# Optimization experiments

Measured on AMD Instinct MI355X. Metric: run time of the kernel, lower is better.

## Reference

```python
import jax, jax.numpy as jnp
import numpy as np

B, C, D = 1024, 1000, 256
EPS = 1e-4


def setup_inputs() -> dict:
    key = jax.random.key(0)
    k_z, k_mu = jax.random.split(key)
    z = jax.random.normal(k_z, (B, D), dtype=jnp.float32)
    mu = jax.random.normal(k_mu, (C, D), dtype=jnp.float32)  # init.normal_(mu, 0, 1)
    prior_logits = jnp.zeros((C,), dtype=jnp.float32)          # init.zeros_
    precision_factor = jnp.eye(D, dtype=jnp.float32)           # init.eye_
    return {"z": z, "mu": mu, "prior_logits": prior_logits,
            "precision_factor": precision_factor}


def reference(z, mu, prior_logits, precision_factor):
    # Shared precision matrix: symmetrized F F^T + eps I  -> (D, D)
    precision = precision_factor @ precision_factor.T
    precision = 0.5 * (precision + precision.T)
    precision = precision + EPS * jnp.eye(D, dtype=precision_factor.dtype)

    log_prior = jax.nn.log_softmax(prior_logits)  # (C,)

    # Mahalanobis distance per (sample, class): (z-mu)^T P (z-mu)
    diff = z[:, None, :] - mu[None, :, :]                      # (B, C, D)
    m2 = jnp.einsum('bcd,de,bce->bc', diff, precision, diff)   # (B, C)

    return log_prior[None, :] - 0.5 * m2
```

## Files before the change

### kernel.cpp

```cpp
#include <hip/hip_runtime.h>
#include <hip/hip_bf16.h>
#include <math.h>

constexpr int Bn = 1024;
constexpr int Cn = 1000;
constexpr int Dn = 256;
constexpr float EPS = 1e-4f;

typedef __attribute__((ext_vector_type(8))) short bf16x8;
typedef __attribute__((ext_vector_type(4))) float f32x4;

static __device__ __forceinline__ unsigned short f2bf(float x) {
    union { float f; unsigned u; } v; v.f = x;
    return (unsigned short)((v.u + 0x7fffu + ((v.u >> 16) & 1u)) >> 16);
}
static __device__ __forceinline__ float bf2f(unsigned short h) {
    union { unsigned u; float f; } v; v.u = ((unsigned)h) << 16; return v.f;
}
static __device__ __forceinline__ bf16x8 cvt8(const float4 lo, const float4 hi) {
    bf16x8 r;
    r[0] = (short)f2bf(lo.x); r[1] = (short)f2bf(lo.y);
    r[2] = (short)f2bf(lo.z); r[3] = (short)f2bf(lo.w);
    r[4] = (short)f2bf(hi.x); r[5] = (short)f2bf(hi.y);
    r[6] = (short)f2bf(hi.z); r[7] = (short)f2bf(hi.w);
    return r;
}

__global__ __launch_bounds__(256) void w_kernel(const float* __restrict__ z,
                                                const float* __restrict__ mu,
                                                const float* __restrict__ logits,
                                                const float* __restrict__ F,
                                                unsigned short* __restrict__ Wb,
                                                float* __restrict__ epsn,
                                                float* __restrict__ lse_p) {
    const int bid = blockIdx.x, tid = threadIdx.x;

    if (bid == 256) {
        __shared__ float rl[256];
        float mx = -INFINITY;
        for (int i = tid; i < Cn; i += 256) mx = fmaxf(mx, logits[i]);
        rl[tid] = mx; __syncthreads();
        for (int s = 128; s > 0; s >>= 1) {
            if (tid < s) rl[tid] = fmaxf(rl[tid], rl[tid + s]);
            __syncthreads();
        }
        mx = rl[0]; __syncthreads();
        float sm = 0.f;
        for (int i = tid; i < Cn; i += 256) sm += expf(logits[i] - mx);
        rl[tid] = sm; __syncthreads();
        for (int s = 128; s > 0; s >>= 1) {
            if (tid < s) rl[tid] += rl[tid + s];
            __syncthreads();
        }
        if (tid == 0) *lse_p = mx + logf(rl[0]);
        return;
    }

    const int row0 = (bid >> 3) * 64;
    const int col0 = (bid & 7) * 32;
    const int lane = tid & 63, w = tid >> 6;
    const int wr = (w >> 1) * 32, wc = (w & 1) * 16;
    const int la = lane & 15, kg = lane >> 4;

    const int g0 = row0 + wr + la;
    const int g1 = g0 + 16;
    const float* arow0 = (g0 < 1024) ? &z[(size_t)g0 * Dn]
                                     : &mu[(size_t)min(g0 - 1024, Cn - 1) * Dn];
    const float* arow1 = (g1 < 1024) ? &z[(size_t)g1 * Dn]
                                     : &mu[(size_t)min(g1 - 1024, Cn - 1) * Dn];
    const int bcol = col0 + wc + la;

    f32x4 acc0 = {0.f, 0.f, 0.f, 0.f};
    f32x4 acc1 = {0.f, 0.f, 0.f, 0.f};

#pragma unroll
    for (int kt = 0; kt < 8; ++kt) {
        const int k0 = kt * 32 + kg * 8;
        const float4 a0lo = *(const float4*)&arow0[k0];
        const float4 a0hi = *(const float4*)&arow0[k0 + 4];
        const float4 a1lo = *(const float4*)&arow1[k0];
        const float4 a1hi = *(const float4*)&arow1[k0 + 4];
        bf16x8 b0;
#pragma unroll
        for (int j = 0; j < 8; ++j)
            b0[j] = (short)f2bf(F[(size_t)(k0 + j) * Dn + bcol]);
        const bf16x8 a0 = cvt8(a0lo, a0hi);
        const bf16x8 a1 = cvt8(a1lo, a1hi);
        acc0 = __builtin_amdgcn_mfma_f32_16x16x32_bf16(a0, b0, acc0, 0, 0, 0);
        acc1 = __builtin_amdgcn_mfma_f32_16x16x32_bf16(a1, b0, acc1, 0, 0, 0);
    }

    const int rb0 = row0 + wr + kg * 4;
#pragma unroll
    for (int j = 0; j < 4; ++j) {
        Wb[(size_t)(rb0 + j) * Dn + bcol]      = f2bf(acc0[j]);
        Wb[(size_t)(rb0 + 16 + j) * Dn + bcol] = f2bf(acc1[j]);
    }

    if (col0 == 0) {
        __shared__ float red[64][4];
        const int r = tid >> 2, q = tid & 3;
        const int g = row0 + r;
        const float* src = (g < 1024) ? &z[(size_t)g * Dn]
                                      : &mu[(size_t)min(g - 1024, Cn - 1) * Dn];
        const float4* p4 = (const float4*)&src[q << 6];
        float s = 0.f;
#pragma unroll
        for (int i = 0; i < 16; ++i) {
            const float4 v = p4[i];
            s += v.x * v.x + v.y * v.y + v.z * v.z + v.w * v.w;
        }
        red[r][q] = s;
        __syncthreads();
        if (tid < 64)
            epsn[row0 + tid] = EPS * (red[tid][0] + red[tid][1] +
                                      red[tid][2] + red[tid][3]);
    }
}

__global__ __launch_bounds__(256) void main_kernel(const unsigned short* __restrict__ Wb,
                                                   const float* __restrict__ epsn,
                                                   const float* __restrict__ logits,
                                                   const float* __restrict__ lse_p,
                                                   float* __restrict__ out) {
    __shared__ float red[64][4];
    __shared__ float rowbias[64], colbias[64];
    const int bid = blockIdx.x, tid = threadIdx.x;
    const int row0 = (bid >> 4) * 64;
    const int col0 = (bid & 15) * 64;
    const int r = tid >> 2, q = tid & 3;

    {
        const bf16x8* py = (const bf16x8*)&Wb[(size_t)(row0 + r) * Dn + (q << 6)];
        float s = 0.f;
#pragma unroll
        for (int i = 0; i < 8; ++i) {
            const bf16x8 h = py[i];
#pragma unroll
            for (int j = 0; j < 8; ++j) {
                const float f = bf2f((unsigned short)h[j]);
                s = fmaf(f, f, s);
            }
        }
        red[r][q] = s;
    }
    __syncthreads();
    if (tid < 64)
        rowbias[tid] = -0.5f * (red[tid][0] + red[tid][1] + red[tid][2] +
                                red[tid][3] + epsn[row0 + tid]);
    __syncthreads();
    {
        const bf16x8* pu = (const bf16x8*)&Wb[(size_t)(1024 + col0 + r) * Dn + (q << 6)];
        float s = 0.f;
#pragma unroll
        for (int i = 0; i < 8; ++i) {
            const bf16x8 h = pu[i];
#pragma unroll
            for (int j = 0; j < 8; ++j) {
                const float f = bf2f((unsigned short)h[j]);
                s = fmaf(f, f, s);
            }
        }
        red[r][q] = s;
    }
    __syncthreads();
    if (tid < 64) {
        const int c = col0 + tid;
        colbias[tid] = (c < Cn)
            ? logits[c] - *lse_p - 0.5f * (red[tid][0] + red[tid][1] + red[tid][2] +
                                           red[tid][3] + epsn[1024 + c])
            : 0.f;
    }
    __syncthreads();

    const int lane = tid & 63, w = tid >> 6;
    const int wr = (w >> 1) * 32, wc = (w & 1) * 32;
    const int la = lane & 15, kg = lane >> 4;

    const bf16x8* pa = (const bf16x8*)&Wb[(size_t)(row0 + wr + la) * Dn + kg * 8];
    const bf16x8* pb = (const bf16x8*)&Wb[(size_t)(1024 + col0 + wc + la) * Dn + kg * 8];

    f32x4 acc00 = {0.f, 0.f, 0.f, 0.f};
    f32x4 acc01 = {0.f, 0.f, 0.f, 0.f};
    f32x4 acc10 = {0.f, 0.f, 0.f, 0.f};
    f32x4 acc11 = {0.f, 0.f, 0.f, 0.f};

#pragma unroll
    for (int kt = 0; kt < 8; ++kt) {
        const bf16x8 a0 = pa[kt * 4];
        const bf16x8 a1 = pa[kt * 4 + 512];
        const bf16x8 b0 = pb[kt * 4];
        const bf16x8 b1 = pb[kt * 4 + 512];
        acc00 = __builtin_amdgcn_mfma_f32_16x16x32_bf16(a0, b0, acc00, 0, 0, 0);
        acc01 = __builtin_amdgcn_mfma_f32_16x16x32_bf16(a0, b1, acc01, 0, 0, 0);
        acc10 = __builtin_amdgcn_mfma_f32_16x16x32_bf16(a1, b0, acc10, 0, 0, 0);
        acc11 = __builtin_amdgcn_mfma_f32_16x16x32_bf16(a1, b1, acc11, 0, 0, 0);
    }

    const int rbase = kg * 4;
#define EPI(ACC, RF, CF)                                                        \
    do {                                                                        \
        const int gcl = wc + (CF)*16 + la;                                      \
        const int gc  = col0 + gcl;                                             \
        if (gc < Cn) {                                                          \
            const float cb = colbias[gcl];                                      \
            _Pragma("unroll")                                                   \
            for (int j = 0; j < 4; ++j) {                                       \
                const int rlc = wr + (RF)*16 + rbase + j;                       \
                out[(size_t)(row0 + rlc) * Cn + gc] = ACC[j] + rowbias[rlc] + cb; \
            }                                                                   \
        }                                                                       \
    } while (0)

    EPI(acc00, 0, 0); EPI(acc01, 0, 1); EPI(acc10, 1, 0); EPI(acc11, 1, 1);
#undef EPI
}

extern "C" void kernel_launch(void* const* d_in, const int* in_sizes, int n_in,
                              void* d_out, int out_size, void* d_ws, size_t ws_size,
                              hipStream_t stream) {
    const float* z      = (const float*)d_in[0];
    const float* mu     = (const float*)d_in[1];
    const float* logits = (const float*)d_in[2];
    const float* F      = (const float*)d_in[3];
    float* out = (float*)d_out;

    char* ws = (char*)d_ws;
    unsigned short* Wb = (unsigned short*)(ws);
    float* epsn = (float*)(ws + (1 << 20));
    float* lse  = epsn + 2048;

    w_kernel<<<dim3(257), dim3(256), 0, stream>>>(z, mu, logits, F, Wb, epsn, lse);
    main_kernel<<<dim3(256), dim3(256), 0, stream>>>(Wb, epsn, logits, lse, out);
}
```

Measured before the change: 21.44 us.

## Fuse W projection and distance GEMM into one kernel with swizzled LDS tiles

Merges the two-kernel pipeline into a single kernel. Each block loads its 64 z rows and 64 mu rows into XOR-swizzled LDS as bf16, projects both through F into LDS, computes the row and column norms, and runs the final MFMA GEMM from LDS. This removes the second launch, the workspace round trip, and the global sync between stages. In exchange, every block recomputes the F projections and the log-sum-exp redundantly, reading all of F, and uses about 130KB of LDS, which limits occupancy to one block per CU.

```diff
diff --git a/kernel.cpp b/kernel.cpp
--- a/kernel.cpp
+++ b/kernel.cpp
@@ -17,26 +17,33 @@
 static __device__ __forceinline__ float bf2f(unsigned short h) {
     union { unsigned u; float f; } v; v.u = ((unsigned)h) << 16; return v.f;
 }
-static __device__ __forceinline__ bf16x8 cvt8(const float4 lo, const float4 hi) {
-    bf16x8 r;
-    r[0] = (short)f2bf(lo.x); r[1] = (short)f2bf(lo.y);
-    r[2] = (short)f2bf(lo.z); r[3] = (short)f2bf(lo.w);
-    r[4] = (short)f2bf(hi.x); r[5] = (short)f2bf(hi.y);
-    r[6] = (short)f2bf(hi.z); r[7] = (short)f2bf(hi.w);
-    return r;
-}
-
-__global__ __launch_bounds__(256) void w_kernel(const float* __restrict__ z,
-                                                const float* __restrict__ mu,
-                                                const float* __restrict__ logits,
-                                                const float* __restrict__ F,
-                                                unsigned short* __restrict__ Wb,
-                                                float* __restrict__ epsn,
-                                                float* __restrict__ lse_p) {
+
+static __device__ __forceinline__ unsigned short* lds_u(unsigned short* base, int row, int b) {
+    return (unsigned short*)((char*)base + row * 512 + (b ^ ((row & 7) << 4)));
+}
+static __device__ __forceinline__ const unsigned short* lds_c(const unsigned short* base, int row, int b) {
+    return (const unsigned short*)((const char*)base + row * 512 + (b ^ ((row & 7) << 4)));
+}
+
+__global__ __launch_bounds__(256) void lda_one_kernel(const float* __restrict__ z,
+                                                      const float* __restrict__ mu,
+                                                      const float* __restrict__ logits,
+                                                      const float* __restrict__ F,
+                                                      float* __restrict__ out) {
+    __shared__ unsigned short Zl[64 * 256];
+    __shared__ unsigned short Ml[64 * 256];
+    __shared__ unsigned short Yl[64 * 256];
+    __shared__ unsigned short Ul[64 * 256];
+    __shared__ float red[64][4];
+    __shared__ float rowbias[64], colbias[64];
+    __shared__ float rl[256];
+    __shared__ float lse_s;
+
     const int bid = blockIdx.x, tid = threadIdx.x;
-
-    if (bid == 256) {
-        __shared__ float rl[256];
+    const int row0 = (bid >> 4) * 64;
+    const int col0 = (bid & 15) * 64;
+
+    {
         float mx = -INFINITY;
         for (int i = tid; i < Cn; i += 256) mx = fmaxf(mx, logits[i]);
         rl[tid] = mx; __syncthreads();
@@ -52,133 +59,117 @@
             if (tid < s) rl[tid] += rl[tid + s];
             __syncthreads();
         }
-        if (tid == 0) *lse_p = mx + logf(rl[0]);
-        return;
-    }
-
-    const int row0 = (bid >> 3) * 64;
-    const int col0 = (bid & 7) * 32;
+        if (tid == 0) lse_s = mx + logf(rl[0]);
+    }
+
+#pragma unroll
+    for (int i = 0; i < 16; ++i) {
+        const int flat = i * 256 + tid;
+        const int r = flat >> 6, c4 = flat & 63;
+        const float4 vz = *(const float4*)&z[(size_t)(row0 + r) * Dn + c4 * 4];
+        ushort4 sz;
+        sz.x = f2bf(vz.x); sz.y = f2bf(vz.y); sz.z = f2bf(vz.z); sz.w = f2bf(vz.w);
+        *(ushort4*)lds_u(Zl, r, c4 * 8) = sz;
+        const int rm = min(col0 + r, Cn - 1);
+        const float4 vm = *(const float4*)&mu[(size_t)rm * Dn + c4 * 4];
+        ushort4 smv;
+        smv.x = f2bf(vm.x); smv.y = f2bf(vm.y); smv.z = f2bf(vm.z); smv.w = f2bf(vm.w);
+        *(ushort4*)lds_u(Ml, r, c4 * 8) = smv;
+    }
+    __syncthreads();
+
     const int lane = tid & 63, w = tid >> 6;
-    const int wr = (w >> 1) * 32, wc = (w & 1) * 16;
     const int la = lane & 15, kg = lane >> 4;
 
-    const int g0 = row0 + wr + la;
-    const int g1 = g0 + 16;
-    const float* arow0 = (g0 < 1024) ? &z[(size_t)g0 * Dn]
-                                     : &mu[(size_t)min(g0 - 1024, Cn - 1) * Dn];
-    const float* arow1 = (g1 < 1024) ? &z[(size_t)g1 * Dn]
-                                     : &mu[(size_t)min(g1 - 1024, Cn - 1) * Dn];
-    const int bcol = col0 + wc + la;
-
-    f32x4 acc0 = {0.f, 0.f, 0.f, 0.f};
-    f32x4 acc1 = {0.f, 0.f, 0.f, 0.f};
-
-#pragma unroll
-    for (int kt = 0; kt < 8; ++kt) {
-        const int k0 = kt * 32 + kg * 8;
-        const float4 a0lo = *(const float4*)&arow0[k0];
-        const float4 a0hi = *(const float4*)&arow0[k0 + 4];
-        const float4 a1lo = *(const float4*)&arow1[k0];
-        const float4 a1hi = *(const float4*)&arow1[k0 + 4];
-        bf16x8 b0;
-#pragma unroll
-        for (int j = 0; j < 8; ++j)
-            b0[j] = (short)f2bf(F[(size_t)(k0 + j) * Dn + bcol]);
-        const bf16x8 a0 = cvt8(a0lo, a0hi);
-        const bf16x8 a1 = cvt8(a1lo, a1hi);
-        acc0 = __builtin_amdgcn_mfma_f32_16x16x32_bf16(a0, b0, acc0, 0, 0, 0);
-        acc1 = __builtin_amdgcn_mfma_f32_16x16x32_bf16(a1, b0, acc1, 0, 0, 0);
-    }
-
-    const int rb0 = row0 + wr + kg * 4;
-#pragma unroll
-    for (int j = 0; j < 4; ++j) {
-        Wb[(size_t)(rb0 + j) * Dn + bcol]      = f2bf(acc0[j]);
-        Wb[(size_t)(rb0 + 16 + j) * Dn + bcol] = f2bf(acc1[j]);
-    }
-
-    if (col0 == 0) {
-        __shared__ float red[64][4];
+    {
+        const int wr = (w >> 1) * 32, wc = (w & 1) * 16;
+#pragma unroll 1
+        for (int ct = 0; ct < 8; ++ct) {
+            const int bcol = ct * 32 + wc + la;
+            bf16x8 ball[8];
+#pragma unroll
+            for (int kt = 0; kt < 8; ++kt) {
+                const int k0 = kt * 32 + kg * 8;
+                float bf[8];
+#pragma unroll
+                for (int j = 0; j < 8; ++j) bf[j] = F[(size_t)(k0 + j) * Dn + bcol];
+                bf16x8 bb;
+#pragma unroll
+                for (int j = 0; j < 8; ++j) bb[j] = (short)f2bf(bf[j]);
+                ball[kt] = bb;
+            }
+#pragma unroll
+            for (int t = 0; t < 2; ++t) {
+                const unsigned short* src = t ? Ml : Zl;
+                unsigned short* dst = t ? Ul : Yl;
+                f32x4 acc0 = {0.f, 0.f, 0.f, 0.f};
+                f32x4 acc1 = {0.f, 0.f, 0.f, 0.f};
+#pragma unroll
+                for (int kt = 0; kt < 8; ++kt) {
+                    const int kb = (kt * 32 + kg * 8) * 2;
+                    const bf16x8 a0 = *(const bf16x8*)lds_c(src, wr + la, kb);
+                    const bf16x8 a1 = *(const bf16x8*)lds_c(src, wr + 16 + la, kb);
+                    acc0 = __builtin_amdgcn_mfma_f32_16x16x32_bf16(a0, ball[kt], acc0, 0, 0, 0);
+                    acc1 = __builtin_amdgcn_mfma_f32_16x16x32_bf16(a1, ball[kt], acc1, 0, 0, 0);
+                }
+                const int rb0 = wr + kg * 4;
+#pragma unroll
+                for (int j = 0; j < 4; ++j) {
+                    *lds_u(dst, rb0 + j, bcol * 2)      = f2bf(acc0[j]);
+                    *lds_u(dst, rb0 + 16 + j, bcol * 2) = f2bf(acc1[j]);
+                }
+            }
+        }
+    }
+    __syncthreads();
+
+    {
         const int r = tid >> 2, q = tid & 3;
-        const int g = row0 + r;
-        const float* src = (g < 1024) ? &z[(size_t)g * Dn]
-                                      : &mu[(size_t)min(g - 1024, Cn - 1) * Dn];
-        const float4* p4 = (const float4*)&src[q << 6];
-        float s = 0.f;
-#pragma unroll
-        for (int i = 0; i < 16; ++i) {
-            const float4 v = p4[i];
-            s += v.x * v.x + v.y * v.y + v.z * v.z + v.w * v.w;
-        }
-        red[r][q] = s;
+        float sy = 0.f, sz2 = 0.f;
+#pragma unroll
+        for (int i = 0; i < 8; ++i) {
+            const bf16x8 hy = *(const bf16x8*)lds_c(Yl, r, q * 128 + i * 16);
+            const bf16x8 hz = *(const bf16x8*)lds_c(Zl, r, q * 128 + i * 16);
+#pragma unroll
+            for (int j = 0; j < 8; ++j) {
+                const float fy = bf2f((unsigned short)hy[j]);
+                const float fz = bf2f((unsigned short)hz[j]);
+                sy = fmaf(fy, fy, sy);
+                sz2 = fmaf(fz, fz, sz2);
+            }
+        }
+        red[r][q] = sy + EPS * sz2;
         __syncthreads();
         if (tid < 64)
-            epsn[row0 + tid] = EPS * (red[tid][0] + red[tid][1] +
-                                      red[tid][2] + red[tid][3]);
-    }
-}
-
-__global__ __launch_bounds__(256) void main_kernel(const unsigned short* __restrict__ Wb,
-                                                   const float* __restrict__ epsn,
-                                                   const float* __restrict__ logits,
-                                                   const float* __restrict__ lse_p,
-                                                   float* __restrict__ out) {
-    __shared__ float red[64][4];
-    __shared__ float rowbias[64], colbias[64];
-    const int bid = blockIdx.x, tid = threadIdx.x;
-    const int row0 = (bid >> 4) * 64;
-    const int col0 = (bid & 15) * 64;
-    const int r = tid >> 2, q = tid & 3;
-
-    {
-        const bf16x8* py = (const bf16x8*)&Wb[(size_t)(row0 + r) * Dn + (q << 6)];
-        float s = 0.f;
+            rowbias[tid] = -0.5f * (red[tid][0] + red[tid][1] + red[tid][2] + red[tid][3]);
+        __syncthreads();
+
+        float su = 0.f, sm2 = 0.f;
 #pragma unroll
         for (int i = 0; i < 8; ++i) {
-            const bf16x8 h = py[i];
+            const bf16x8 hu = *(const bf16x8*)lds_c(Ul, r, q * 128 + i * 16);
+            const bf16x8 hm = *(const bf16x8*)lds_c(Ml, r, q * 128 + i * 16);
 #pragma unroll
             for (int j = 0; j < 8; ++j) {
-                const float f = bf2f((unsigned short)h[j]);
-                s = fmaf(f, f, s);
-            }
-        }
-        red[r][q] = s;
-    }
-    __syncthreads();
-    if (tid < 64)
-        rowbias[tid] = -0.5f * (red[tid][0] + red[tid][1] + red[tid][2] +
-                                red[tid][3] + epsn[row0 + tid]);
-    __syncthreads();
-    {
-        const bf16x8* pu = (const bf16x8*)&Wb[(size_t)(1024 + col0 + r) * Dn + (q << 6)];
-        float s = 0.f;
-#pragma unroll
-        for (int i = 0; i < 8; ++i) {
-            const bf16x8 h = pu[i];
-#pragma unroll
-            for (int j = 0; j < 8; ++j) {
-                const float f = bf2f((unsigned short)h[j]);
-                s = fmaf(f, f, s);
-            }
-        }
-        red[r][q] = s;
-    }
-    __syncthreads();
-    if (tid < 64) {
-        const int c = col0 + tid;
-        colbias[tid] = (c < Cn)
-            ? logits[c] - *lse_p - 0.5f * (red[tid][0] + red[tid][1] + red[tid][2] +
-                                           red[tid][3] + epsn[1024 + c])
-            : 0.f;
-    }
-    __syncthreads();
-
-    const int lane = tid & 63, w = tid >> 6;
-    const int wr = (w >> 1) * 32, wc = (w & 1) * 32;
-    const int la = lane & 15, kg = lane >> 4;
-
-    const bf16x8* pa = (const bf16x8*)&Wb[(size_t)(row0 + wr + la) * Dn + kg * 8];
-    const bf16x8* pb = (const bf16x8*)&Wb[(size_t)(1024 + col0 + wc + la) * Dn + kg * 8];
+                const float fu = bf2f((unsigned short)hu[j]);
+                const float fm = bf2f((unsigned short)hm[j]);
+                su = fmaf(fu, fu, su);
+                sm2 = fmaf(fm, fm, sm2);
+            }
+        }
+        red[r][q] = su + EPS * sm2;
+        __syncthreads();
+        if (tid < 64) {
+            const int c = col0 + tid;
+            colbias[tid] = (c < Cn)
+                ? logits[c] - lse_s - 0.5f * (red[tid][0] + red[tid][1] +
+                                              red[tid][2] + red[tid][3])
+                : 0.f;
+        }
+        __syncthreads();
+    }
+
+    const int wr2 = (w >> 1) * 32, wc2 = (w & 1) * 32;
 
     f32x4 acc00 = {0.f, 0.f, 0.f, 0.f};
     f32x4 acc01 = {0.f, 0.f, 0.f, 0.f};
@@ -187,10 +178,11 @@
 
 #pragma unroll
     for (int kt = 0; kt < 8; ++kt) {
-        const bf16x8 a0 = pa[kt * 4];
-        const bf16x8 a1 = pa[kt * 4 + 512];
-        const bf16x8 b0 = pb[kt * 4];
-        const bf16x8 b1 = pb[kt * 4 + 512];
+        const int kb = (kt * 32 + kg * 8) * 2;
+        const bf16x8 a0 = *(const bf16x8*)lds_c(Yl, wr2 + la, kb);
+        const bf16x8 a1 = *(const bf16x8*)lds_c(Yl, wr2 + 16 + la, kb);
+        const bf16x8 b0 = *(const bf16x8*)lds_c(Ul, wc2 + la, kb);
+        const bf16x8 b1 = *(const bf16x8*)lds_c(Ul, wc2 + 16 + la, kb);
         acc00 = __builtin_amdgcn_mfma_f32_16x16x32_bf16(a0, b0, acc00, 0, 0, 0);
         acc01 = __builtin_amdgcn_mfma_f32_16x16x32_bf16(a0, b1, acc01, 0, 0, 0);
         acc10 = __builtin_amdgcn_mfma_f32_16x16x32_bf16(a1, b0, acc10, 0, 0, 0);
@@ -200,13 +192,13 @@
     const int rbase = kg * 4;
 #define EPI(ACC, RF, CF)                                                        \
     do {                                                                        \
-        const int gcl = wc + (CF)*16 + la;                                      \
+        const int gcl = wc2 + (CF)*16 + la;                                     \
         const int gc  = col0 + gcl;                                             \
         if (gc < Cn) {                                                          \
             const float cb = colbias[gcl];                                      \
             _Pragma("unroll")                                                   \
             for (int j = 0; j < 4; ++j) {                                       \
-                const int rlc = wr + (RF)*16 + rbase + j;                       \
+                const int rlc = wr2 + (RF)*16 + rbase + j;                      \
                 out[(size_t)(row0 + rlc) * Cn + gc] = ACC[j] + rowbias[rlc] + cb; \
             }                                                                   \
         }                                                                       \
@@ -225,11 +217,5 @@
     const float* F      = (const float*)d_in[3];
     float* out = (float*)d_out;
 
-    char* ws = (char*)d_ws;
-    unsigned short* Wb = (unsigned short*)(ws);
-    float* epsn = (float*)(ws + (1 << 20));
-    float* lse  = epsn + 2048;
-
-    w_kernel<<<dim3(257), dim3(256), 0, stream>>>(z, mu, logits, F, Wb, epsn, lse);
-    main_kernel<<<dim3(256), dim3(256), 0, stream>>>(Wb, epsn, logits, lse, out);
-}
+    lda_one_kernel<<<dim3(256), dim3(256), 0, stream>>>(z, mu, logits, F, out);
+}
```

Measured after the change: 40.85 us. +90.5%, slower.
